# Kernel tuning notes

Measured on AMD Instinct MI355X. Metric: run time of the kernel, lower is better.

The kernel has to match this reference:

```python
import jax, jax.numpy as jnp
import numpy as np
from jax import lax

RADIUS = 2
DILATION = 2
KS = 2 * RADIUS + 1  # 5
PERM = np.array([6, 8, 1, 11, 2, 10, 0, 7, 9, 4, 5, 3])


def _shift_kernels():
    # Reproduce the torch index construction in numpy (all constants).
    six = np.array([[0, 1, 1], [1, 1, 0], [1, 0, 1], [1, 1, 2], [2, 1, 1], [1, 2, 1]])
    # pairwise squared distances between the 6 neighbourhood offsets
    d = ((six[:, None, :] - six[None, :, :]) ** 2).sum(-1)
    x, y = np.meshgrid(np.arange(6), np.arange(6), indexing='ij')
    mask = (x > y).reshape(-1) & (d == 2).reshape(-1)
    idx1 = np.repeat(six[:, None, :], 6, axis=1).reshape(-1, 3)[mask]
    idx2 = np.repeat(six[None, :, :], 6, axis=0).reshape(-1, 3)[mask]
    k1 = np.zeros((12, 1, 3, 3, 3), np.float32)
    k2 = np.zeros((12, 1, 3, 3, 3), np.float32)
    r = np.arange(12)
    k1[r, 0, idx1[:, 0], idx1[:, 1], idx1[:, 2]] = 1.0
    k2[r, 0, idx2[:, 0], idx2[:, 1], idx2[:, 2]] = 1.0
    return jnp.asarray(k1), jnp.asarray(k2)

_K1, _K2 = _shift_kernels()
DN = ('NCDHW', 'OIDHW', 'NCDHW')


def _rep_pad(x, p):
    return jnp.pad(x, ((0, 0), (0, 0), (p, p), (p, p), (p, p)), mode='edge')


def mindssc(img):
    # img: [N,1,D,H,W]
    p1 = _rep_pad(img, DILATION)
    c1 = lax.conv_general_dilated(p1, _K1, (1, 1, 1), 'VALID',
                                  rhs_dilation=(DILATION,) * 3, dimension_numbers=DN)
    c2 = lax.conv_general_dilated(p1, _K2, (1, 1, 1), 'VALID',
                                  rhs_dilation=(DILATION,) * 3, dimension_numbers=DN)
    diff2 = (c1 - c2) ** 2  # [N,12,D,H,W]
    p2 = _rep_pad(diff2, RADIUS)
    ssd = lax.reduce_window(p2, 0.0, lax.add, (1, 1, KS, KS, KS),
                            (1, 1, 1, 1, 1), 'VALID') / float(KS ** 3)
    mind = ssd - jnp.min(ssd, axis=1, keepdims=True)
    mind_var = jnp.mean(mind, axis=1, keepdims=True)
    m = jnp.mean(mind_var)
    mind_var = jnp.clip(mind_var, m * 0.001, m * 1000.0)
    mind = jnp.exp(-mind / mind_var)
    return mind[:, PERM]


def setup_inputs() -> dict:
    key = jax.random.key(0)
    k1, k2 = jax.random.split(key)
    shape = (1, 1, 128, 128, 128)
    return {
        'y_true': jax.random.normal(k1, shape, dtype=jnp.float32),
        'y_pred': jax.random.normal(k2, shape, dtype=jnp.float32),
    }


def reference(y_true, y_pred):
    return jnp.mean((mindssc(y_pred) - mindssc(y_true)) ** 2)
```

## Files before the change

### kernel.cpp

```cpp
#include <hip/hip_runtime.h>

#define DIM   128
#define DMASK 127
#define PLANE (DIM * DIM)
#define VOX   (1 << 21)
#define NCH   12

#define CHS   (VOX + 2048)
#define IMGS  (NCH * CHS + 1024)

typedef __attribute__((ext_vector_type(2))) _Float16 half2v;
typedef __attribute__((ext_vector_type(4))) _Float16 half4v;

__constant__ int c_sd1[12] = { 0, 0, 0, 0, 0, 2, 2, 2, 0, 0, 0, 0};
__constant__ int c_sh1[12] = { 0,-2,-2, 0, 0, 0, 0, 0, 2, 2, 2, 2};
__constant__ int c_sw1[12] = {-2, 0, 0, 2, 2, 0, 0, 0, 0, 0, 0, 0};
__constant__ int c_sd2[12] = {-2,-2, 0,-2, 0, 0, 0, 0,-2, 0, 0, 2};
__constant__ int c_sh2[12] = { 0, 0, 0, 0,-2, 0,-2, 0, 0, 0, 0, 0};
__constant__ int c_sw2[12] = { 0, 0,-2, 0, 0,-2, 0, 2, 0,-2, 2, 0};

__device__ __forceinline__ int clamp7(int v) { return min(max(v, 0), DMASK); }

__global__ __launch_bounds__(256, 3) void f123(const float* __restrict__ img0,
                                               const float* __restrict__ img1,
                                               _Float16* __restrict__ Sall) {
    const float* img = blockIdx.y ? img1 : img0;
    _Float16* outS = Sall + (size_t)blockIdx.y * IMGS;
    const char* imgc = (const char*)img;

    int wid = (blockIdx.x << 2) + (threadIdx.x >> 6);
    int ch = wid >> 7;
    int hs = (wid >> 3) & 15;
    int ds = wid & 7;
    int h0 = hs << 3;
    int d0 = ds << 4;
    int l  = threadIdx.x & 63;

    int sd1 = c_sd1[ch], sh1 = c_sh1[ch], sw1 = c_sw1[ch];
    int sd2 = c_sd2[ch], sh2 = c_sh2[ch], sw2 = c_sw2[ch];

    int rowOffA[12], rowOffB[12];
#pragma unroll
    for (int r = 0; r < 12; ++r) {
        int hq = clamp7(h0 - 2 + r);
        rowOffA[r] = clamp7(hq + sh1) * (DIM * 4);
        rowOffB[r] = clamp7(hq + sh2) * (DIM * 4);
    }

    int c2 = l << 1;
    int colA = min(max(c2 + sw1, 0), 126) * 4;
    int colB = min(max(c2 + sw2, 0), 126) * 4;
    bool fixAlo = (sw1 < 0) && (l == 0);
    bool fixAhi = (sw1 > 0) && (l == 63);
    bool fixBlo = (sw2 < 0) && (l == 0);
    bool fixBhi = (sw2 > 0) && (l == 63);

    float2 win[8];
    half2v hist[5][8];
#pragma unroll
    for (int k = 0; k < 8; ++k) {
        win[k].x = 0.0f; win[k].y = 0.0f;
#pragma unroll
        for (int s = 0; s < 5; ++s) hist[s][k] = half2v{(_Float16)0.0f, (_Float16)0.0f};
    }

    _Float16* dstBase = outS + (size_t)ch * CHS + h0 * DIM + c2;

    for (int oo = 0; oo < 4; ++oo) {
#pragma unroll
        for (int s5 = 0; s5 < 5; ++s5) {
            int it = oo * 5 + s5;
            int dp = clamp7(d0 - 2 + it);
            int pOffA = clamp7(dp + sd1) * (PLANE * 4);
            int pOffB = clamp7(dp + sd2) * (PLANE * 4);

            float tX[12], tY[12];
#pragma unroll
            for (int r = 0; r < 12; ++r) {
                float2 a = *(const float2*)(imgc + (pOffA + rowOffA[r] + colA));
                float2 b = *(const float2*)(imgc + (pOffB + rowOffB[r] + colB));
                a.y = fixAlo ? a.x : a.y;  a.x = fixAhi ? a.y : a.x;
                b.y = fixBlo ? b.x : b.y;  b.x = fixBhi ? b.y : b.x;
                float dx = a.x - b.x; dx *= dx;
                float dy = a.y - b.y; dy *= dy;
                float lx = __shfl_up(dx, 1, 64);
                float ly = __shfl_up(dy, 1, 64);
                float rx = __shfl_down(dx, 1, 64);
                float ry = __shfl_down(dy, 1, 64);
                ly = (l == 0)  ? dx : ly;
                rx = (l == 63) ? dy : rx;
                tX[r] = lx + ly + dx + dy + rx;
                tY[r] = ly + dx + dy + rx + ry;
            }

            float sx = tX[0] + tX[1] + tX[2] + tX[3] + tX[4];
            float sy = tY[0] + tY[1] + tY[2] + tY[3] + tY[4];
            bool dowrite = (it >= 4);
            _Float16* dstD = dstBase + (size_t)(d0 + it - 4) * PLANE;
#pragma unroll
            for (int k = 0; k < 8; ++k) {
                half2v hv = { (_Float16)sx, (_Float16)sy };
                half2v old = hist[s5][k];
                win[k].x += (float)hv[0] - (float)old[0];
                win[k].y += (float)hv[1] - (float)old[1];
                hist[s5][k] = hv;
                if (dowrite) {
                    half2v ov = { (_Float16)win[k].x, (_Float16)win[k].y };
                    *(half2v*)(dstD + k * DIM) = ov;
                }
                if (k < 7) {
                    sx += tX[k + 5] - tX[k];
                    sy += tY[k + 5] - tY[k];
                }
            }
        }
    }
}

__global__ __launch_bounds__(256, 3) void kmse(const _Float16* __restrict__ S0,
                                               const _Float16* __restrict__ S1,
                                               float* __restrict__ partial) {
    int t = blockIdx.x * 256 + threadIdx.x;

    half4v v0[NCH], v1[NCH];
#pragma unroll
    for (int ch = 0; ch < NCH; ++ch)
        v0[ch] = ((const half4v*)(S0 + (size_t)ch * CHS))[t];
#pragma unroll
    for (int ch = 0; ch < NCH; ++ch)
        v1[ch] = ((const half4v*)(S1 + (size_t)ch * CHS))[t];

    float mn0[4], sm0[4], mn1[4], sm1[4];
#pragma unroll
    for (int j = 0; j < 4; ++j) {
        mn0[j] = 3.4e38f; sm0[j] = 0.0f;
        mn1[j] = 3.4e38f; sm1[j] = 0.0f;
    }
#pragma unroll
    for (int ch = 0; ch < NCH; ++ch)
#pragma unroll
        for (int j = 0; j < 4; ++j) {
            float s0 = (float)v0[ch][j];
            float s1 = (float)v1[ch][j];
            mn0[j] = fminf(mn0[j], s0); sm0[j] += s0;
            mn1[j] = fminf(mn1[j], s1); sm1[j] += s1;
        }

    float inv0[4], inv1[4];
#pragma unroll
    for (int j = 0; j < 4; ++j) {
        inv0[j] = __fdividef(1.0f, sm0[j] * (1.0f / 12.0f) - mn0[j]);
        inv1[j] = __fdividef(1.0f, sm1[j] * (1.0f / 12.0f) - mn1[j]);
    }

    float acc = 0.0f;
#pragma unroll
    for (int ch = 0; ch < NCH; ++ch)
#pragma unroll
        for (int j = 0; j < 4; ++j) {
            float e0 = __expf(-((float)v0[ch][j] - mn0[j]) * inv0[j]);
            float e1 = __expf(-((float)v1[ch][j] - mn1[j]) * inv1[j]);
            float df = e0 - e1;
            acc += df * df;
        }

#pragma unroll
    for (int off = 32; off > 0; off >>= 1)
        acc += __shfl_down(acc, off, 64);
    __shared__ float smem[4];
    int lane = threadIdx.x & 63, wv = threadIdx.x >> 6;
    if (lane == 0) smem[wv] = acc;
    __syncthreads();
    if (threadIdx.x == 0)
        partial[blockIdx.x] = smem[0] + smem[1] + smem[2] + smem[3];
}

__global__ __launch_bounds__(256) void kred(const float* __restrict__ partial,
                                            float* __restrict__ out) {
    int tid = threadIdx.x;
    float acc = 0.0f;
#pragma unroll
    for (int k = 0; k < 8; ++k)
        acc += partial[tid + (k << 8)];
#pragma unroll
    for (int off = 32; off > 0; off >>= 1)
        acc += __shfl_down(acc, off, 64);
    __shared__ float smem[4];
    int lane = tid & 63, wv = tid >> 6;
    if (lane == 0) smem[wv] = acc;
    __syncthreads();
    if (tid == 0)
        out[0] = (smem[0] + smem[1] + smem[2] + smem[3])
               * (1.0f / (12.0f * (float)VOX));
}

__global__ void kdiag(float* out, float ws_mb) { out[0] = ws_mb; }

extern "C" void kernel_launch(void* const* d_in, const int* in_sizes, int n_in,
                              void* d_out, int out_size, void* d_ws, size_t ws_size,
                              hipStream_t stream) {
    const float* y_true = (const float*)d_in[0];
    const float* y_pred = (const float*)d_in[1];
    float* out = (float*)d_out;

    const size_t NEED = 2ull * IMGS * sizeof(_Float16) + 8192 + 64;
    if (ws_size < NEED) {
        kdiag<<<1, 1, 0, stream>>>(out, (float)(ws_size >> 20));
        return;
    }

    _Float16* S0      = (_Float16*)d_ws;
    _Float16* S1      = S0 + (size_t)IMGS;
    float*    partial = (float*)(S1 + (size_t)IMGS);

    f123<<<dim3(384, 2), 256, 0, stream>>>(y_true, y_pred, S0);
    kmse<<<VOX / 4 / 256, 256, 0, stream>>>(S0, S1, partial);
    kred<<<1, 256, 0, stream>>>(partial, out);
}
```

Measured before the change: 131.4 us.

## Halve depth tile per wave, double occupancy, widen MSE kernel to 8 voxels

The stencil kernel now gives each wave 8 output depth slices instead of 16. It launches twice as many blocks with a higher occupancy target, and the depth loop is fully unrolled, so latency hiding improves at the cost of more halo recomputation (12 input planes for 8 outputs instead of 20 for 16). The MSE kernel handles 8 voxels per thread with 16-byte loads and processes the two images one after the other, holding the first image's exponentials as fp16 to limit register pressure. The final reduction now sums 1024 partials to match. Storing the exponentials in fp16 adds a small precision loss.

```diff
diff --git a/kernel.cpp b/kernel.cpp
--- a/kernel.cpp
+++ b/kernel.cpp
@@ -10,7 +10,7 @@
 #define IMGS  (NCH * CHS + 1024)
 
 typedef __attribute__((ext_vector_type(2))) _Float16 half2v;
-typedef __attribute__((ext_vector_type(4))) _Float16 half4v;
+typedef __attribute__((ext_vector_type(8))) _Float16 half8v;
 
 __constant__ int c_sd1[12] = { 0, 0, 0, 0, 0, 2, 2, 2, 0, 0, 0, 0};
 __constant__ int c_sh1[12] = { 0,-2,-2, 0, 0, 0, 0, 0, 2, 2, 2, 2};
@@ -21,7 +21,7 @@
 
 __device__ __forceinline__ int clamp7(int v) { return min(max(v, 0), DMASK); }
 
-__global__ __launch_bounds__(256, 3) void f123(const float* __restrict__ img0,
+__global__ __launch_bounds__(256, 6) void f123(const float* __restrict__ img0,
                                                const float* __restrict__ img1,
                                                _Float16* __restrict__ Sall) {
     const float* img = blockIdx.y ? img1 : img0;
@@ -29,11 +29,11 @@
     const char* imgc = (const char*)img;
 
     int wid = (blockIdx.x << 2) + (threadIdx.x >> 6);
-    int ch = wid >> 7;
-    int hs = (wid >> 3) & 15;
-    int ds = wid & 7;
+    int ch = wid >> 8;
+    int hs = (wid >> 4) & 15;
+    int ds = wid & 15;
     int h0 = hs << 3;
-    int d0 = ds << 4;
+    int d0 = ds << 3;
     int l  = threadIdx.x & 63;
 
     int sd1 = c_sd1[ch], sh1 = c_sh1[ch], sw1 = c_sw1[ch];
@@ -66,52 +66,50 @@
 
     _Float16* dstBase = outS + (size_t)ch * CHS + h0 * DIM + c2;
 
-    for (int oo = 0; oo < 4; ++oo) {
-#pragma unroll
-        for (int s5 = 0; s5 < 5; ++s5) {
-            int it = oo * 5 + s5;
-            int dp = clamp7(d0 - 2 + it);
-            int pOffA = clamp7(dp + sd1) * (PLANE * 4);
-            int pOffB = clamp7(dp + sd2) * (PLANE * 4);
-
-            float tX[12], tY[12];
-#pragma unroll
-            for (int r = 0; r < 12; ++r) {
-                float2 a = *(const float2*)(imgc + (pOffA + rowOffA[r] + colA));
-                float2 b = *(const float2*)(imgc + (pOffB + rowOffB[r] + colB));
-                a.y = fixAlo ? a.x : a.y;  a.x = fixAhi ? a.y : a.x;
-                b.y = fixBlo ? b.x : b.y;  b.x = fixBhi ? b.y : b.x;
-                float dx = a.x - b.x; dx *= dx;
-                float dy = a.y - b.y; dy *= dy;
-                float lx = __shfl_up(dx, 1, 64);
-                float ly = __shfl_up(dy, 1, 64);
-                float rx = __shfl_down(dx, 1, 64);
-                float ry = __shfl_down(dy, 1, 64);
-                ly = (l == 0)  ? dx : ly;
-                rx = (l == 63) ? dy : rx;
-                tX[r] = lx + ly + dx + dy + rx;
-                tY[r] = ly + dx + dy + rx + ry;
+#pragma unroll
+    for (int it = 0; it < 12; ++it) {
+        const int s5 = it % 5;
+        int dp = clamp7(d0 - 2 + it);
+        int pOffA = clamp7(dp + sd1) * (PLANE * 4);
+        int pOffB = clamp7(dp + sd2) * (PLANE * 4);
+
+        float tX[12], tY[12];
+#pragma unroll
+        for (int r = 0; r < 12; ++r) {
+            float2 a = *(const float2*)(imgc + (pOffA + rowOffA[r] + colA));
+            float2 b = *(const float2*)(imgc + (pOffB + rowOffB[r] + colB));
+            a.y = fixAlo ? a.x : a.y;  a.x = fixAhi ? a.y : a.x;
+            b.y = fixBlo ? b.x : b.y;  b.x = fixBhi ? b.y : b.x;
+            float dx = a.x - b.x; dx *= dx;
+            float dy = a.y - b.y; dy *= dy;
+            float lx = __shfl_up(dx, 1, 64);
+            float ly = __shfl_up(dy, 1, 64);
+            float rx = __shfl_down(dx, 1, 64);
+            float ry = __shfl_down(dy, 1, 64);
+            ly = (l == 0)  ? dx : ly;
+            rx = (l == 63) ? dy : rx;
+            tX[r] = lx + ly + dx + dy + rx;
+            tY[r] = ly + dx + dy + rx + ry;
+        }
+
+        float sx = tX[0] + tX[1] + tX[2] + tX[3] + tX[4];
+        float sy = tY[0] + tY[1] + tY[2] + tY[3] + tY[4];
+        bool dowrite = (it >= 4);
+        _Float16* dstD = dstBase + (size_t)(d0 + it - 4) * PLANE;
+#pragma unroll
+        for (int k = 0; k < 8; ++k) {
+            half2v hv = { (_Float16)sx, (_Float16)sy };
+            half2v old = hist[s5][k];
+            win[k].x += (float)hv[0] - (float)old[0];
+            win[k].y += (float)hv[1] - (float)old[1];
+            hist[s5][k] = hv;
+            if (dowrite) {
+                half2v ov = { (_Float16)win[k].x, (_Float16)win[k].y };
+                *(half2v*)(dstD + k * DIM) = ov;
             }
-
-            float sx = tX[0] + tX[1] + tX[2] + tX[3] + tX[4];
-            float sy = tY[0] + tY[1] + tY[2] + tY[3] + tY[4];
-            bool dowrite = (it >= 4);
-            _Float16* dstD = dstBase + (size_t)(d0 + it - 4) * PLANE;
-#pragma unroll
-            for (int k = 0; k < 8; ++k) {
-                half2v hv = { (_Float16)sx, (_Float16)sy };
-                half2v old = hist[s5][k];
-                win[k].x += (float)hv[0] - (float)old[0];
-                win[k].y += (float)hv[1] - (float)old[1];
-                hist[s5][k] = hv;
-                if (dowrite) {
-                    half2v ov = { (_Float16)win[k].x, (_Float16)win[k].y };
-                    *(half2v*)(dstD + k * DIM) = ov;
-                }
-                if (k < 7) {
-                    sx += tX[k + 5] - tX[k];
-                    sy += tY[k + 5] - tY[k];
-                }
+            if (k < 7) {
+                sx += tX[k + 5] - tX[k];
+                sy += tY[k + 5] - tY[k];
             }
         }
     }
@@ -122,45 +120,58 @@
                                                float* __restrict__ partial) {
     int t = blockIdx.x * 256 + threadIdx.x;
 
-    half4v v0[NCH], v1[NCH];
-#pragma unroll
-    for (int ch = 0; ch < NCH; ++ch)
-        v0[ch] = ((const half4v*)(S0 + (size_t)ch * CHS))[t];
-#pragma unroll
-    for (int ch = 0; ch < NCH; ++ch)
-        v1[ch] = ((const half4v*)(S1 + (size_t)ch * CHS))[t];
-
-    float mn0[4], sm0[4], mn1[4], sm1[4];
-#pragma unroll
-    for (int j = 0; j < 4; ++j) {
-        mn0[j] = 3.4e38f; sm0[j] = 0.0f;
-        mn1[j] = 3.4e38f; sm1[j] = 0.0f;
-    }
-#pragma unroll
-    for (int ch = 0; ch < NCH; ++ch)
-#pragma unroll
-        for (int j = 0; j < 4; ++j) {
-            float s0 = (float)v0[ch][j];
-            float s1 = (float)v1[ch][j];
-            mn0[j] = fminf(mn0[j], s0); sm0[j] += s0;
-            mn1[j] = fminf(mn1[j], s1); sm1[j] += s1;
-        }
-
-    float inv0[4], inv1[4];
-#pragma unroll
-    for (int j = 0; j < 4; ++j) {
-        inv0[j] = __fdividef(1.0f, sm0[j] * (1.0f / 12.0f) - mn0[j]);
-        inv1[j] = __fdividef(1.0f, sm1[j] * (1.0f / 12.0f) - mn1[j]);
-    }
+    float mn[8], sm[8];
+    half8v v[NCH];
+
+#pragma unroll
+    for (int ch = 0; ch < NCH; ++ch)
+        v[ch] = ((const half8v*)(S0 + (size_t)ch * CHS))[t];
+#pragma unroll
+    for (int j = 0; j < 8; ++j) { mn[j] = 3.4e38f; sm[j] = 0.0f; }
+#pragma unroll
+    for (int ch = 0; ch < NCH; ++ch)
+#pragma unroll
+        for (int j = 0; j < 8; ++j) {
+            float s = (float)v[ch][j];
+            mn[j] = fminf(mn[j], s); sm[j] += s;
+        }
+    float inv[8];
+#pragma unroll
+    for (int j = 0; j < 8; ++j)
+        inv[j] = __fdividef(1.0f, sm[j] * (1.0f / 12.0f) - mn[j]);
+    half8v e0[NCH];
+#pragma unroll
+    for (int ch = 0; ch < NCH; ++ch) {
+        half8v e;
+#pragma unroll
+        for (int j = 0; j < 8; ++j)
+            e[j] = (_Float16)__expf(-((float)v[ch][j] - mn[j]) * inv[j]);
+        e0[ch] = e;
+    }
+
+#pragma unroll
+    for (int ch = 0; ch < NCH; ++ch)
+        v[ch] = ((const half8v*)(S1 + (size_t)ch * CHS))[t];
+#pragma unroll
+    for (int j = 0; j < 8; ++j) { mn[j] = 3.4e38f; sm[j] = 0.0f; }
+#pragma unroll
+    for (int ch = 0; ch < NCH; ++ch)
+#pragma unroll
+        for (int j = 0; j < 8; ++j) {
+            float s = (float)v[ch][j];
+            mn[j] = fminf(mn[j], s); sm[j] += s;
+        }
+#pragma unroll
+    for (int j = 0; j < 8; ++j)
+        inv[j] = __fdividef(1.0f, sm[j] * (1.0f / 12.0f) - mn[j]);
 
     float acc = 0.0f;
 #pragma unroll
     for (int ch = 0; ch < NCH; ++ch)
 #pragma unroll
-        for (int j = 0; j < 4; ++j) {
-            float e0 = __expf(-((float)v0[ch][j] - mn0[j]) * inv0[j]);
-            float e1 = __expf(-((float)v1[ch][j] - mn1[j]) * inv1[j]);
-            float df = e0 - e1;
+        for (int j = 0; j < 8; ++j) {
+            float e1 = __expf(-((float)v[ch][j] - mn[j]) * inv[j]);
+            float df = (float)e0[ch][j] - e1;
             acc += df * df;
         }
 
@@ -178,10 +189,8 @@
 __global__ __launch_bounds__(256) void kred(const float* __restrict__ partial,
                                             float* __restrict__ out) {
     int tid = threadIdx.x;
-    float acc = 0.0f;
-#pragma unroll
-    for (int k = 0; k < 8; ++k)
-        acc += partial[tid + (k << 8)];
+    float acc = partial[tid] + partial[tid + 256]
+              + partial[tid + 512] + partial[tid + 768];
 #pragma unroll
     for (int off = 32; off > 0; off >>= 1)
         acc += __shfl_down(acc, off, 64);
@@ -213,7 +222,7 @@
     _Float16* S1      = S0 + (size_t)IMGS;
     float*    partial = (float*)(S1 + (size_t)IMGS);
 
-    f123<<<dim3(384, 2), 256, 0, stream>>>(y_true, y_pred, S0);
-    kmse<<<VOX / 4 / 256, 256, 0, stream>>>(S0, S1, partial);
+    f123<<<dim3(768, 2), 256, 0, stream>>>(y_true, y_pred, S0);
+    kmse<<<VOX / 8 / 256, 256, 0, stream>>>(S0, S1, partial);
     kred<<<1, 256, 0, stream>>>(partial, out);
 }
```

After: 440.2 us. 235% more time.

## Fuse SSD box filter and MIND/MSE reduction into one kernel via shared memory

Applied to the files above, without the earlier changes.

Merges the box-filter kernel and the per-voxel MIND/MSE kernel into one kernel. Each 768-thread block handles an 8-deep by 8-row tile with all 12 channels and both images, staging the box-filtered values in LDS instead of writing half-precision volumes to global memory. This removes the large global write and read-back of the intermediate SSD volumes and one kernel launch. In exchange it adds two block barriers per depth slice, leaves a third of the threads idle during the exp phase, and recomputes halo planes (12 planes loaded for 8 outputs) instead of the previous 20 for 16. The running window becomes a direct 5-term sum over the history registers, and the grid drops to 256 blocks, which may limit occupancy and latency hiding.

```diff
diff --git a/kernel.cpp b/kernel.cpp
--- a/kernel.cpp
+++ b/kernel.cpp
@@ -6,11 +6,7 @@
 #define VOX   (1 << 21)
 #define NCH   12
 
-#define CHS   (VOX + 2048)
-#define IMGS  (NCH * CHS + 1024)
-
 typedef __attribute__((ext_vector_type(2))) _Float16 half2v;
-typedef __attribute__((ext_vector_type(4))) _Float16 half4v;
 
 __constant__ int c_sd1[12] = { 0, 0, 0, 0, 0, 2, 2, 2, 0, 0, 0, 0};
 __constant__ int c_sh1[12] = { 0,-2,-2, 0, 0, 0, 0, 0, 2, 2, 2, 2};
@@ -21,23 +17,21 @@
 
 __device__ __forceinline__ int clamp7(int v) { return min(max(v, 0), DMASK); }
 
-__global__ __launch_bounds__(256, 3) void f123(const float* __restrict__ img0,
-                                               const float* __restrict__ img1,
-                                               _Float16* __restrict__ Sall) {
-    const float* img = blockIdx.y ? img1 : img0;
-    _Float16* outS = Sall + (size_t)blockIdx.y * IMGS;
-    const char* imgc = (const char*)img;
-
-    int wid = (blockIdx.x << 2) + (threadIdx.x >> 6);
-    int ch = wid >> 7;
-    int hs = (wid >> 3) & 15;
-    int ds = wid & 7;
-    int h0 = hs << 3;
-    int d0 = ds << 4;
-    int l  = threadIdx.x & 63;
-
-    int sd1 = c_sd1[ch], sh1 = c_sh1[ch], sw1 = c_sw1[ch];
-    int sd2 = c_sd2[ch], sh2 = c_sh2[ch], sw2 = c_sw2[ch];
+__global__ __launch_bounds__(768, 3) void fmega(const float* __restrict__ img0,
+                                                const float* __restrict__ img1,
+                                                float* __restrict__ partial) {
+    int bx = blockIdx.x;
+    int h0 = (bx & 15) << 3;
+    int d0 = (bx >> 4) << 3;
+    int tid = threadIdx.x;
+    int w  = tid >> 6;
+    int l  = tid & 63;
+
+    __shared__ _Float16 sbuf[24 * 1024];
+    __shared__ float rsm[12];
+
+    int sd1 = c_sd1[w], sh1 = c_sh1[w], sw1 = c_sw1[w];
+    int sd2 = c_sd2[w], sh2 = c_sh2[w], sw2 = c_sw2[w];
 
     int rowOffA[12], rowOffB[12];
 #pragma unroll
@@ -55,30 +49,33 @@
     bool fixBlo = (sw2 < 0) && (l == 0);
     bool fixBhi = (sw2 > 0) && (l == 63);
 
-    float2 win[8];
-    half2v hist[5][8];
-#pragma unroll
-    for (int k = 0; k < 8; ++k) {
-        win[k].x = 0.0f; win[k].y = 0.0f;
-#pragma unroll
-        for (int s = 0; s < 5; ++s) hist[s][k] = half2v{(_Float16)0.0f, (_Float16)0.0f};
-    }
-
-    _Float16* dstBase = outS + (size_t)ch * CHS + h0 * DIM + c2;
-
-    for (int oo = 0; oo < 4; ++oo) {
-#pragma unroll
-        for (int s5 = 0; s5 < 5; ++s5) {
-            int it = oo * 5 + s5;
-            int dp = clamp7(d0 - 2 + it);
-            int pOffA = clamp7(dp + sd1) * (PLANE * 4);
-            int pOffB = clamp7(dp + sd2) * (PLANE * 4);
-
+    half2v hist[2][5][8];
+#pragma unroll
+    for (int i = 0; i < 2; ++i)
+#pragma unroll
+        for (int s = 0; s < 5; ++s)
+#pragma unroll
+            for (int k = 0; k < 8; ++k)
+                hist[i][s][k] = half2v{(_Float16)0.0f, (_Float16)0.0f};
+
+    const char* ic[2] = { (const char*)img0, (const char*)img1 };
+    float acc = 0.0f;
+
+#pragma unroll
+    for (int it = 0; it < 12; ++it) {
+        const int s5 = it % 5;
+        int dp = clamp7(d0 - 2 + it);
+        int pOffA = clamp7(dp + sd1) * (PLANE * 4);
+        int pOffB = clamp7(dp + sd2) * (PLANE * 4);
+
+#pragma unroll
+        for (int i = 0; i < 2; ++i) {
+            const char* im = ic[i];
             float tX[12], tY[12];
 #pragma unroll
             for (int r = 0; r < 12; ++r) {
-                float2 a = *(const float2*)(imgc + (pOffA + rowOffA[r] + colA));
-                float2 b = *(const float2*)(imgc + (pOffB + rowOffB[r] + colB));
+                float2 a = *(const float2*)(im + (pOffA + rowOffA[r] + colA));
+                float2 b = *(const float2*)(im + (pOffB + rowOffB[r] + colB));
                 a.y = fixAlo ? a.x : a.y;  a.x = fixAhi ? a.y : a.x;
                 b.y = fixBlo ? b.x : b.y;  b.x = fixBhi ? b.y : b.x;
                 float dx = a.x - b.x; dx *= dx;
@@ -92,96 +89,88 @@
                 tX[r] = lx + ly + dx + dy + rx;
                 tY[r] = ly + dx + dy + rx + ry;
             }
-
             float sx = tX[0] + tX[1] + tX[2] + tX[3] + tX[4];
             float sy = tY[0] + tY[1] + tY[2] + tY[3] + tY[4];
-            bool dowrite = (it >= 4);
-            _Float16* dstD = dstBase + (size_t)(d0 + it - 4) * PLANE;
 #pragma unroll
             for (int k = 0; k < 8; ++k) {
-                half2v hv = { (_Float16)sx, (_Float16)sy };
-                half2v old = hist[s5][k];
-                win[k].x += (float)hv[0] - (float)old[0];
-                win[k].y += (float)hv[1] - (float)old[1];
-                hist[s5][k] = hv;
-                if (dowrite) {
-                    half2v ov = { (_Float16)win[k].x, (_Float16)win[k].y };
-                    *(half2v*)(dstD + k * DIM) = ov;
-                }
+                hist[i][s5][k] = half2v{ (_Float16)sx, (_Float16)sy };
                 if (k < 7) {
                     sx += tX[k + 5] - tX[k];
                     sy += tY[k + 5] - tY[k];
                 }
             }
         }
-    }
-}
-
-__global__ __launch_bounds__(256, 3) void kmse(const _Float16* __restrict__ S0,
-                                               const _Float16* __restrict__ S1,
-                                               float* __restrict__ partial) {
-    int t = blockIdx.x * 256 + threadIdx.x;
-
-    half4v v0[NCH], v1[NCH];
-#pragma unroll
-    for (int ch = 0; ch < NCH; ++ch)
-        v0[ch] = ((const half4v*)(S0 + (size_t)ch * CHS))[t];
-#pragma unroll
-    for (int ch = 0; ch < NCH; ++ch)
-        v1[ch] = ((const half4v*)(S1 + (size_t)ch * CHS))[t];
-
-    float mn0[4], sm0[4], mn1[4], sm1[4];
-#pragma unroll
-    for (int j = 0; j < 4; ++j) {
-        mn0[j] = 3.4e38f; sm0[j] = 0.0f;
-        mn1[j] = 3.4e38f; sm1[j] = 0.0f;
-    }
-#pragma unroll
-    for (int ch = 0; ch < NCH; ++ch)
-#pragma unroll
-        for (int j = 0; j < 4; ++j) {
-            float s0 = (float)v0[ch][j];
-            float s1 = (float)v1[ch][j];
-            mn0[j] = fminf(mn0[j], s0); sm0[j] += s0;
-            mn1[j] = fminf(mn1[j], s1); sm1[j] += s1;
+
+        if (it >= 4) {
+#pragma unroll
+            for (int i = 0; i < 2; ++i) {
+                half2v* dst = (half2v*)sbuf + ((w << 1) + i) * 512 + l;
+#pragma unroll
+                for (int k = 0; k < 8; ++k) {
+                    float wx = 0.0f, wy = 0.0f;
+#pragma unroll
+                    for (int s = 0; s < 5; ++s) {
+                        wx += (float)hist[i][s][k][0];
+                        wy += (float)hist[i][s][k][1];
+                    }
+                    dst[k * 64] = half2v{ (_Float16)wx, (_Float16)wy };
+                }
+            }
+            __syncthreads();
+
+            if (tid < 512) {
+                half2v sA[NCH], sB[NCH];
+#pragma unroll
+                for (int ch = 0; ch < NCH; ++ch) {
+                    sA[ch] = ((half2v*)sbuf)[((ch << 1) + 0) * 512 + tid];
+                    sB[ch] = ((half2v*)sbuf)[((ch << 1) + 1) * 512 + tid];
+                }
+                float mnA0 = 3.4e38f, smA0 = 0.0f, mnA1 = 3.4e38f, smA1 = 0.0f;
+                float mnB0 = 3.4e38f, smB0 = 0.0f, mnB1 = 3.4e38f, smB1 = 0.0f;
+#pragma unroll
+                for (int ch = 0; ch < NCH; ++ch) {
+                    float a0 = (float)sA[ch][0], a1 = (float)sA[ch][1];
+                    float b0 = (float)sB[ch][0], b1 = (float)sB[ch][1];
+                    mnA0 = fminf(mnA0, a0); smA0 += a0;
+                    mnA1 = fminf(mnA1, a1); smA1 += a1;
+                    mnB0 = fminf(mnB0, b0); smB0 += b0;
+                    mnB1 = fminf(mnB1, b1); smB1 += b1;
+                }
+                float iA0 = __fdividef(1.0f, smA0 * (1.0f / 12.0f) - mnA0);
+                float iA1 = __fdividef(1.0f, smA1 * (1.0f / 12.0f) - mnA1);
+                float iB0 = __fdividef(1.0f, smB0 * (1.0f / 12.0f) - mnB0);
+                float iB1 = __fdividef(1.0f, smB1 * (1.0f / 12.0f) - mnB1);
+#pragma unroll
+                for (int ch = 0; ch < NCH; ++ch) {
+                    float e00 = __expf(-((float)sA[ch][0] - mnA0) * iA0);
+                    float e10 = __expf(-((float)sB[ch][0] - mnB0) * iB0);
+                    float df0 = e00 - e10; acc += df0 * df0;
+                    float e01 = __expf(-((float)sA[ch][1] - mnA1) * iA1);
+                    float e11 = __expf(-((float)sB[ch][1] - mnB1) * iB1);
+                    float df1 = e01 - e11; acc += df1 * df1;
+                }
+            }
+            __syncthreads();
         }
-
-    float inv0[4], inv1[4];
-#pragma unroll
-    for (int j = 0; j < 4; ++j) {
-        inv0[j] = __fdividef(1.0f, sm0[j] * (1.0f / 12.0f) - mn0[j]);
-        inv1[j] = __fdividef(1.0f, sm1[j] * (1.0f / 12.0f) - mn1[j]);
-    }
-
-    float acc = 0.0f;
-#pragma unroll
-    for (int ch = 0; ch < NCH; ++ch)
-#pragma unroll
-        for (int j = 0; j < 4; ++j) {
-            float e0 = __expf(-((float)v0[ch][j] - mn0[j]) * inv0[j]);
-            float e1 = __expf(-((float)v1[ch][j] - mn1[j]) * inv1[j]);
-            float df = e0 - e1;
-            acc += df * df;
-        }
+    }
 
 #pragma unroll
     for (int off = 32; off > 0; off >>= 1)
         acc += __shfl_down(acc, off, 64);
-    __shared__ float smem[4];
-    int lane = threadIdx.x & 63, wv = threadIdx.x >> 6;
-    if (lane == 0) smem[wv] = acc;
+    if (l == 0) rsm[w] = acc;
     __syncthreads();
-    if (threadIdx.x == 0)
-        partial[blockIdx.x] = smem[0] + smem[1] + smem[2] + smem[3];
+    if (tid == 0) {
+        float t = 0.0f;
+#pragma unroll
+        for (int i = 0; i < 12; ++i) t += rsm[i];
+        partial[bx] = t;
+    }
 }
 
 __global__ __launch_bounds__(256) void kred(const float* __restrict__ partial,
                                             float* __restrict__ out) {
     int tid = threadIdx.x;
-    float acc = 0.0f;
-#pragma unroll
-    for (int k = 0; k < 8; ++k)
-        acc += partial[tid + (k << 8)];
+    float acc = partial[tid];
 #pragma unroll
     for (int off = 32; off > 0; off >>= 1)
         acc += __shfl_down(acc, off, 64);
@@ -203,17 +192,14 @@
     const float* y_pred = (const float*)d_in[1];
     float* out = (float*)d_out;
 
-    const size_t NEED = 2ull * IMGS * sizeof(_Float16) + 8192 + 64;
+    const size_t NEED = 4096;
     if (ws_size < NEED) {
         kdiag<<<1, 1, 0, stream>>>(out, (float)(ws_size >> 20));
         return;
     }
 
-    _Float16* S0      = (_Float16*)d_ws;
-    _Float16* S1      = S0 + (size_t)IMGS;
-    float*    partial = (float*)(S1 + (size_t)IMGS);
-
-    f123<<<dim3(384, 2), 256, 0, stream>>>(y_true, y_pred, S0);
-    kmse<<<VOX / 4 / 256, 256, 0, stream>>>(S0, S1, partial);
-    kred<<<1, 256, 0, stream>>>(partial, out);
+    float* partial = (float*)d_ws;
+
+    fmega<<<256, 768, 0, stream>>>(y_true, y_pred, partial);
+    kred <<<1, 256, 0, stream>>>(partial, out);
 }
```

After: 275.3 us. +109.5%, slower.
